# Optimization experiments

Hardware: AMD Instinct MI355X
Metric: run time of the kernel (lower is better)

## Reference

```python
import jax, jax.numpy as jnp
import numpy as np

EPS = 1e-8  # F.cosine_similarity default eps


def setup_inputs() -> dict:
    key = jax.random.key(0)
    k1, k2, k3 = jax.random.split(key, 3)
    C, S, Q, D_IN, Z_DIM = 256, 5, 64, 1024, 128
    xs = jax.random.normal(k1, (C, S, D_IN), dtype=jnp.float32)
    xq = jax.random.normal(k2, (C, Q, D_IN), dtype=jnp.float32)
    W = jax.random.normal(k3, (D_IN, Z_DIM), dtype=jnp.float32) / np.sqrt(D_IN)
    return {"xs": xs, "xq": xq, "W": W}


def _protonet_loss(xs, xq, W):
    C, S, D = xs.shape
    Q = xq.shape[1]
    # encoder (linear) applied to concatenated support+query, as in the original
    x = jnp.concatenate([xs.reshape(C * S, D), xq.reshape(C * Q, D)], axis=0)
    z = x @ W                                   # [C*(S+Q), Zd]
    Zd = z.shape[-1]
    z_proto = z[: C * S].reshape(C, S, Zd).mean(axis=1)   # [C, Zd]
    zq = z[C * S:]                                        # [C*Q, Zd]
    # squared euclidean distance (GEMM form, avoids [CQ, C, Zd] intermediate)
    d2 = (jnp.sum(zq * zq, axis=-1, keepdims=True)
          + jnp.sum(z_proto * z_proto, axis=-1)[None, :]
          - 2.0 * (zq @ z_proto.T))                       # [C*Q, C]
    lp = d2.reshape(C, Q, C)                              # label_predicts
    # leave-one-out: for each class i drop column i -> [C, Q, C-1]
    loo_idx = np.stack([np.delete(np.arange(C), i) for i in range(C)])  # [C, C-1]
    idx = jnp.broadcast_to(jnp.asarray(loo_idx)[:, None, :], (C, Q, C - 1))
    loo = jnp.take_along_axis(lp, idx, axis=2)            # [C, Q, C-1]
    # pairwise cosine similarity between query rows j<k, per class
    nrm = jnp.maximum(jnp.linalg.norm(loo, axis=-1), EPS)
    a = loo / nrm[..., None]
    sim = jnp.einsum('cqd,ckd->cqk', a, a)                # [C, Q, Q]
    pair_mask = jnp.triu(jnp.ones((Q, Q), dtype=bool), 1)
    n_pairs = C * (Q * (Q - 1) // 2)
    cos_loss = jnp.sum(jnp.where(pair_mask[None], sim, 0.0)) / n_pairs
    # log_softmax over prototype axis; accuracy vs diagonal targets
    log_p_y = jax.nn.log_softmax(-d2, axis=1).reshape(C, Q, C)
    y_hat = jnp.argmax(log_p_y, axis=2)                   # [C, Q]
    acc = jnp.mean((y_hat == jnp.arange(C)[:, None]).astype(jnp.float32))
    # original overwrites loss_val with the cosine-similarity loss
    return cos_loss, acc


def reference(xs, xq, W):
    return _protonet_loss(xs, xq, W)
```

## Files before the change

kernel.cpp:

```cpp
#include <hip/hip_runtime.h>


typedef __attribute__((ext_vector_type(8))) short s8v;
typedef __attribute__((ext_vector_type(4))) float f32x4;

__device__ __forceinline__ short f2bf(float f) {
  union { float f; unsigned u; } v; v.f = f;
  unsigned r = (v.u + 0x7fffu + ((v.u >> 16) & 1u)) >> 16;
  return (short)r;
}

__global__ __launch_bounds__(256) void k_prep(
    const float* __restrict__ xs, const float* __restrict__ W,
    float* __restrict__ xbar, unsigned short* __restrict__ Wt,
    float* __restrict__ out) {
  __shared__ unsigned short T[128 * 68];
  const int tid = threadIdx.x;
  if (blockIdx.x < 256) {
    const int c = blockIdx.x;
    if (c == 0 && tid < 2) out[tid] = 0.0f;
    const float* b = xs + (size_t)c * 5120;
    for (int e = tid; e < 1024; e += 256) {
      float s = b[e] + b[1024 + e] + b[2048 + e] + b[3072 + e] + b[4096 + e];
      xbar[(size_t)c * 1024 + e] = s * 0.2f;
    }
  } else {
    const int kb = (blockIdx.x - 256) * 64;
#pragma unroll
    for (int s = 0; s < 8; ++s) {
      int idx = tid + s * 256;
      int kr = idx >> 5, n4 = idx & 31;
      float4 v = *(const float4*)(W + (size_t)(kb + kr) * 128 + n4 * 4);
      T[(n4 * 4 + 0) * 68 + kr] = (unsigned short)f2bf(v.x);
      T[(n4 * 4 + 1) * 68 + kr] = (unsigned short)f2bf(v.y);
      T[(n4 * 4 + 2) * 68 + kr] = (unsigned short)f2bf(v.z);
      T[(n4 * 4 + 3) * 68 + kr] = (unsigned short)f2bf(v.w);
    }
    __syncthreads();
#pragma unroll
    for (int s = 0; s < 8; ++s) {
      int idx = tid + s * 256;
      int n = idx >> 4, k4 = idx & 15;
      ushort4 o;
      o.x = T[n * 68 + k4 * 4 + 0];
      o.y = T[n * 68 + k4 * 4 + 1];
      o.z = T[n * 68 + k4 * 4 + 2];
      o.w = T[n * 68 + k4 * 4 + 3];
      *(ushort4*)(Wt + (size_t)n * 1024 + kb + k4 * 4) = o;
    }
  }
}

__global__ __launch_bounds__(256) void k_gemm_z(
    const float* __restrict__ xbar, const float* __restrict__ xq,
    const unsigned short* __restrict__ Wt,
    unsigned short* __restrict__ zb, float* __restrict__ n2) {
  __shared__ float R[4][16][132];
  const int tid = threadIdx.x;
  const int w = tid >> 6, l = tid & 63, ln = l & 15, qd = l >> 4;
  const int rb = blockIdx.x * 16;
  const float* abase = (rb < 256) ? (xbar + (size_t)rb * 1024)
                                  : (xq + (size_t)(rb - 256) * 1024);
  const float* arow = abase + (size_t)ln * 1024 + w * 256 + qd * 8;
  const unsigned short* bbase = Wt + (size_t)ln * 1024 + w * 256 + qd * 8;

  f32x4 acc[8] = {};
  float4 a0c = *(const float4*)(arow + 0);
  float4 a1c = *(const float4*)(arow + 4);
  s8v bc[8];
#pragma unroll
  for (int t = 0; t < 8; ++t)
    bc[t] = *(const s8v*)(bbase + (size_t)t * 16384);

#pragma unroll
  for (int kt = 0; kt < 8; ++kt) {
    float4 a0n, a1n;
    s8v bn[8];
    if (kt < 7) {
      a0n = *(const float4*)(arow + (kt + 1) * 32);
      a1n = *(const float4*)(arow + (kt + 1) * 32 + 4);
#pragma unroll
      for (int t = 0; t < 8; ++t)
        bn[t] = *(const s8v*)(bbase + (size_t)t * 16384 + (kt + 1) * 32);
    }
    s8v af = { f2bf(a0c.x), f2bf(a0c.y), f2bf(a0c.z), f2bf(a0c.w),
               f2bf(a1c.x), f2bf(a1c.y), f2bf(a1c.z), f2bf(a1c.w) };
#pragma unroll
    for (int t = 0; t < 8; ++t)
      acc[t] = __builtin_amdgcn_mfma_f32_16x16x32_bf16(af, bc[t], acc[t], 0, 0, 0);
    if (kt < 7) {
      a0c = a0n; a1c = a1n;
#pragma unroll
      for (int t = 0; t < 8; ++t) bc[t] = bn[t];
    }
  }

#pragma unroll
  for (int p = 0; p < 4; ++p)
#pragma unroll
    for (int t = 0; t < 8; ++t)
      R[w][qd * 4 + p][t * 16 + ln] = acc[t][p];
  __syncthreads();
  {
    const int r = tid >> 4, cc = (tid & 15) * 8;
    float v[8];
#pragma unroll
    for (int e = 0; e < 8; ++e)
      v[e] = R[0][r][cc + e] + R[1][r][cc + e] + R[2][r][cc + e] + R[3][r][cc + e];
    s8v o = { f2bf(v[0]), f2bf(v[1]), f2bf(v[2]), f2bf(v[3]),
              f2bf(v[4]), f2bf(v[5]), f2bf(v[6]), f2bf(v[7]) };
    const int grow = rb + r;
    *(s8v*)&zb[(size_t)grow * 128 + cc] = o;
    float sp = 0.0f;
#pragma unroll
    for (int e = 0; e < 8; ++e) sp += v[e] * v[e];
    sp += __shfl_xor(sp, 1);
    sp += __shfl_xor(sp, 2);
    sp += __shfl_xor(sp, 4);
    sp += __shfl_xor(sp, 8);
    if ((tid & 15) == 0) n2[grow] = sp;
  }
}

__global__ __launch_bounds__(256, 1) void k_d2red(
    const unsigned short* __restrict__ zb, const float* __restrict__ n2,
    float* __restrict__ out) {
  __shared__ float Dt[256 * 65];
  __shared__ float rv[256];
  __shared__ int   ri[256];
  __shared__ float rss[256];
  __shared__ float invn[64];
  __shared__ float sred[4];
  __shared__ float s_tc, s_aq2, s_corr;
  const int tid = threadIdx.x;
  const int c = blockIdx.x;
  const int w = tid >> 6, lane = tid & 63, ln = lane & 15, qd = lane >> 4;

  f32x4 acc[16] = {};
  const unsigned short* Az = zb + (size_t)(256 + c * 64 + w * 16 + ln) * 128;
#pragma unroll
  for (int kt = 0; kt < 4; ++kt) {
    s8v af = *(const s8v*)(Az + kt * 32 + qd * 8);
#pragma unroll
    for (int t = 0; t < 16; ++t) {
      s8v bf = *(const s8v*)(zb + (size_t)(t * 16 + ln) * 128 + kt * 32 + qd * 8);
      acc[t] = __builtin_amdgcn_mfma_f32_16x16x32_bf16(af, bf, acc[t], 0, 0, 0);
    }
  }
#pragma unroll
  for (int p = 0; p < 4; ++p) {
    int qloc = w * 16 + qd * 4 + p;
    float qn = n2[256 + c * 64 + qloc];
#pragma unroll
    for (int t = 0; t < 16; ++t) {
      int j = t * 16 + ln;
      Dt[j * 65 + qloc] = qn + n2[j] - 2.0f * acc[t][p];
    }
  }
  __syncthreads();

  {
    const int q = tid & 63, jb = (tid >> 6) * 64;
    float mn = 3.4e38f; int mi = 0; float ss = 0.0f;
    for (int jj = 0; jj < 64; ++jj) {
      int j = jb + jj;
      float f = Dt[j * 65 + q];
      ss += f * f;
      if (f < mn) { mn = f; mi = j; }
    }
    rv[tid] = mn; ri[tid] = mi; rss[tid] = ss;
  }
  __syncthreads();
  if (tid < 64) {
    float bm = rv[tid]; int bi = ri[tid]; float ss = rss[tid];
    for (int hh = 1; hh < 4; ++hh) {
      float v = rv[hh * 64 + tid];
      ss += rss[hh * 64 + tid];
      if (v < bm) { bm = v; bi = ri[hh * 64 + tid]; }
    }
    float col = Dt[c * 65 + tid];
    float loo2 = fmaxf(ss - col * col, 0.0f);
    float nrm = fmaxf(sqrtf(loo2), 1e-8f);
    float inv = 1.0f / nrm;
    invn[tid] = inv;
    float aq2 = loo2 * inv * inv;
    float corr = (bi == c) ? 1.0f : 0.0f;
    for (int m = 1; m < 64; m <<= 1) {
      aq2 += __shfl_xor(aq2, m);
      corr += __shfl_xor(corr, m);
    }
    if (tid == 0) { s_aq2 = aq2; s_corr = corr; }
  }
  __syncthreads();
  float t = 0.0f;
  for (int qq = 0; qq < 64; ++qq) t += Dt[tid * 65 + qq] * invn[qq];
  if (tid == c) s_tc = t;
  float t2 = t * t;
  for (int m = 1; m < 64; m <<= 1) t2 += __shfl_xor(t2, m);
  if ((tid & 63) == 0) sred[tid >> 6] = t2;
  __syncthreads();
  if (tid == 0) {
    float S2 = sred[0] + sred[1] + sred[2] + sred[3];
    float bs = 0.5f * (S2 - s_tc * s_tc - s_aq2);
    atomicAdd(&out[0], bs * (1.0f / 516096.0f));
    atomicAdd(&out[1], s_corr * (1.0f / 16384.0f));
  }
}

extern "C" void kernel_launch(void* const* d_in, const int* in_sizes, int n_in,
                              void* d_out, int out_size, void* d_ws, size_t ws_size,
                              hipStream_t stream) {
  const float* xs = (const float*)d_in[0];
  const float* xq = (const float*)d_in[1];
  const float* W  = (const float*)d_in[2];
  float* out = (float*)d_out;

  float* ws = (float*)d_ws;
  float* xbar = ws;
  unsigned short* Wt = (unsigned short*)(xbar + 262144);
  unsigned short* zb = Wt + 131072;
  float* n2 = (float*)(zb + (size_t)16640 * 128);

  k_prep<<<dim3(272), dim3(256), 0, stream>>>(xs, W, xbar, Wt, out);
  k_gemm_z<<<dim3(1040), dim3(256), 0, stream>>>(xbar, xq, Wt, zb, n2);
  k_d2red<<<dim3(256), dim3(256), 0, stream>>>(zb, n2, out);
}
```

Before: 152.7 us.

## Split GEMM work across waves by output columns instead of K, drop LDS reduction

```diff
diff --git a/kernel.cpp b/kernel.cpp
--- a/kernel.cpp
+++ b/kernel.cpp
@@ -55,71 +55,44 @@
     const float* __restrict__ xbar, const float* __restrict__ xq,
     const unsigned short* __restrict__ Wt,
     unsigned short* __restrict__ zb, float* __restrict__ n2) {
-  __shared__ float R[4][16][132];
+  __shared__ float P[4][16];
   const int tid = threadIdx.x;
   const int w = tid >> 6, l = tid & 63, ln = l & 15, qd = l >> 4;
   const int rb = blockIdx.x * 16;
   const float* abase = (rb < 256) ? (xbar + (size_t)rb * 1024)
                                   : (xq + (size_t)(rb - 256) * 1024);
-  const float* arow = abase + (size_t)ln * 1024 + w * 256 + qd * 8;
-  const unsigned short* bbase = Wt + (size_t)ln * 1024 + w * 256 + qd * 8;
-
-  f32x4 acc[8] = {};
-  float4 a0c = *(const float4*)(arow + 0);
-  float4 a1c = *(const float4*)(arow + 4);
-  s8v bc[8];
-#pragma unroll
-  for (int t = 0; t < 8; ++t)
-    bc[t] = *(const s8v*)(bbase + (size_t)t * 16384);
-
-#pragma unroll
-  for (int kt = 0; kt < 8; ++kt) {
-    float4 a0n, a1n;
-    s8v bn[8];
-    if (kt < 7) {
-      a0n = *(const float4*)(arow + (kt + 1) * 32);
-      a1n = *(const float4*)(arow + (kt + 1) * 32 + 4);
-#pragma unroll
-      for (int t = 0; t < 8; ++t)
-        bn[t] = *(const s8v*)(bbase + (size_t)t * 16384 + (kt + 1) * 32);
-    }
-    s8v af = { f2bf(a0c.x), f2bf(a0c.y), f2bf(a0c.z), f2bf(a0c.w),
-               f2bf(a1c.x), f2bf(a1c.y), f2bf(a1c.z), f2bf(a1c.w) };
-#pragma unroll
-    for (int t = 0; t < 8; ++t)
-      acc[t] = __builtin_amdgcn_mfma_f32_16x16x32_bf16(af, bc[t], acc[t], 0, 0, 0);
-    if (kt < 7) {
-      a0c = a0n; a1c = a1n;
-#pragma unroll
-      for (int t = 0; t < 8; ++t) bc[t] = bn[t];
-    }
-  }
-
-#pragma unroll
-  for (int p = 0; p < 4; ++p)
-#pragma unroll
-    for (int t = 0; t < 8; ++t)
-      R[w][qd * 4 + p][t * 16 + ln] = acc[t][p];
-  __syncthreads();
-  {
-    const int r = tid >> 4, cc = (tid & 15) * 8;
-    float v[8];
-#pragma unroll
-    for (int e = 0; e < 8; ++e)
-      v[e] = R[0][r][cc + e] + R[1][r][cc + e] + R[2][r][cc + e] + R[3][r][cc + e];
-    s8v o = { f2bf(v[0]), f2bf(v[1]), f2bf(v[2]), f2bf(v[3]),
-              f2bf(v[4]), f2bf(v[5]), f2bf(v[6]), f2bf(v[7]) };
-    const int grow = rb + r;
-    *(s8v*)&zb[(size_t)grow * 128 + cc] = o;
-    float sp = 0.0f;
-#pragma unroll
-    for (int e = 0; e < 8; ++e) sp += v[e] * v[e];
+  const float* arow = abase + (size_t)ln * 1024 + qd * 8;
+  const unsigned short* b0p = Wt + (size_t)(w * 32 + ln) * 1024 + qd * 8;
+  const unsigned short* b1p = b0p + 16 * 1024;
+
+  f32x4 acc0 = {}, acc1 = {};
+#pragma unroll 4
+  for (int kt = 0; kt < 32; ++kt) {
+    float4 a0 = *(const float4*)(arow + kt * 32);
+    float4 a1 = *(const float4*)(arow + kt * 32 + 4);
+    s8v b0 = *(const s8v*)(b0p + kt * 32);
+    s8v b1 = *(const s8v*)(b1p + kt * 32);
+    s8v af = { f2bf(a0.x), f2bf(a0.y), f2bf(a0.z), f2bf(a0.w),
+               f2bf(a1.x), f2bf(a1.y), f2bf(a1.z), f2bf(a1.w) };
+    acc0 = __builtin_amdgcn_mfma_f32_16x16x32_bf16(af, b0, acc0, 0, 0, 0);
+    acc1 = __builtin_amdgcn_mfma_f32_16x16x32_bf16(af, b1, acc1, 0, 0, 0);
+  }
+#pragma unroll
+  for (int p = 0; p < 4; ++p) {
+    const int grow = rb + qd * 4 + p;
+    float v0 = acc0[p], v1 = acc1[p];
+    zb[(size_t)grow * 128 + w * 32 + ln] = (unsigned short)f2bf(v0);
+    zb[(size_t)grow * 128 + w * 32 + 16 + ln] = (unsigned short)f2bf(v1);
+    float sp = v0 * v0 + v1 * v1;
     sp += __shfl_xor(sp, 1);
     sp += __shfl_xor(sp, 2);
     sp += __shfl_xor(sp, 4);
     sp += __shfl_xor(sp, 8);
-    if ((tid & 15) == 0) n2[grow] = sp;
-  }
+    if (ln == 0) P[w][qd * 4 + p] = sp;
+  }
+  __syncthreads();
+  if (tid < 16)
+    n2[rb + tid] = P[0][tid] + P[1][tid] + P[2][tid] + P[3][tid];
 }
 
 __global__ __launch_bounds__(256, 1) void k_d2red(
@@ -138,14 +111,20 @@
 
   f32x4 acc[16] = {};
   const unsigned short* Az = zb + (size_t)(256 + c * 64 + w * 16 + ln) * 128;
-#pragma unroll
-  for (int kt = 0; kt < 4; ++kt) {
-    s8v af = *(const s8v*)(Az + kt * 32 + qd * 8);
-#pragma unroll
-    for (int t = 0; t < 16; ++t) {
-      s8v bf = *(const s8v*)(zb + (size_t)(t * 16 + ln) * 128 + kt * 32 + qd * 8);
-      acc[t] = __builtin_amdgcn_mfma_f32_16x16x32_bf16(af, bf, acc[t], 0, 0, 0);
-    }
+  s8v af[4];
+#pragma unroll
+  for (int kt = 0; kt < 4; ++kt) af[kt] = *(const s8v*)(Az + kt * 32 + qd * 8);
+#pragma unroll
+  for (int t = 0; t < 16; ++t) {
+    const unsigned short* Bz = zb + (size_t)(t * 16 + ln) * 128 + qd * 8;
+    s8v bf0 = *(const s8v*)(Bz + 0 * 32);
+    s8v bf1 = *(const s8v*)(Bz + 1 * 32);
+    s8v bf2 = *(const s8v*)(Bz + 2 * 32);
+    s8v bf3 = *(const s8v*)(Bz + 3 * 32);
+    acc[t] = __builtin_amdgcn_mfma_f32_16x16x32_bf16(af[0], bf0, acc[t], 0, 0, 0);
+    acc[t] = __builtin_amdgcn_mfma_f32_16x16x32_bf16(af[1], bf1, acc[t], 0, 0, 0);
+    acc[t] = __builtin_amdgcn_mfma_f32_16x16x32_bf16(af[2], bf2, acc[t], 0, 0, 0);
+    acc[t] = __builtin_amdgcn_mfma_f32_16x16x32_bf16(af[3], bf3, acc[t], 0, 0, 0);
   }
 #pragma unroll
   for (int p = 0; p < 4; ++p) {
```

After: 178.2 us. 1.17x slower.
